# Kernel tuning notes

Measured on AMD Instinct MI355X. Metric: run time of the kernel, lower is better.

Reference implementation:

```python
import jax, jax.numpy as jnp
import numpy as np

H, HKV, D, HIDDEN = 32, 8, 128, 4096
G = H // HKV  # GQA group size = 4
ROPE_THETA = 10000.0


def fwht(x):
    """Fast Walsh-Hadamard transform over the last axis (scale=1, like faster_hadamard_transform default)."""
    d = x.shape[-1]
    orig = x.shape
    x = x.reshape(-1, d)
    h = 1
    while h < d:
        x = x.reshape(-1, d // (2 * h), 2, h)
        a, b = x[:, :, 0, :], x[:, :, 1, :]
        x = jnp.stack([a + b, a - b], axis=2).reshape(-1, d)
        h *= 2
    return x.reshape(orig)


def rope(x, pos):
    """NeoX-style (rotate-half) RoPE at scalar position `pos`; x: [..., D]."""
    half = D // 2
    inv_freq = 1.0 / (ROPE_THETA ** (jnp.arange(0, D, 2, dtype=jnp.float32) / D))  # [half]
    ang = jnp.float32(pos) * inv_freq
    cos, sin = jnp.cos(ang), jnp.sin(ang)
    x1, x2 = x[..., :half], x[..., half:]
    return jnp.concatenate([x1 * cos - x2 * sin, x2 * cos + x1 * sin], axis=-1)


def quant2bit(x):
    """2-bit quantization of Hadamard-domain vectors: per-vector scale = mean(|x|), codes in {-2,-1,0,1}."""
    s = jnp.mean(jnp.abs(x), axis=-1, keepdims=True) + 1e-6
    code = jnp.clip(jnp.round(x / s), -2.0, 1.0)
    return code, s


def _forward(hidden_states, Wq, Wk, Wv, Wo, k_cache, v_cache, top_k):
    x = hidden_states[0, 0]                                 # [HIDDEN]
    q = (x @ Wq.T).reshape(H, D)
    k = (x @ Wk.T).reshape(HKV, D)
    v = (x @ Wv.T).reshape(HKV, D)
    pos = k_cache.shape[0]                                  # decode position (cache len before append)
    q = rope(q, pos)
    k = rope(k, pos)
    # append to cache -> total T = S + 1 tokens
    K = jnp.concatenate([k_cache, k[None]], axis=0)          # [T, HKV, D]
    V = jnp.concatenate([v_cache, v[None]], axis=0)          # [T, HKV, D]
    T = K.shape[0]
    # Hadamard transform + 2-bit codes for estimation
    hq = fwht(q)                                             # [H, D]
    hK = fwht(K)                                             # [T, HKV, D]
    cq, sq = quant2bit(hq)                                   # [H,D], [H,1]
    ck, sk = quant2bit(hK)                                   # [T,HKV,D], [T,HKV,1]
    # estimated attention scores from low-bit codes, per query head
    est = jnp.einsum('ngd,tnd->ngt', cq.reshape(HKV, G, D), ck).reshape(H, T)
    skh = jnp.repeat(sk[:, :, 0].T, G, axis=0)               # [H, T]
    est = est * sq * skh
    est = est.at[:, -1].set(jnp.inf)                         # always keep the current token
    # top-k index selection per head
    _, idx = jax.lax.top_k(est, top_k)                       # [H, top_k]
    kv_map = jnp.arange(H) // G                              # [H]
    Ksel = K[idx, kv_map[:, None], :]                        # [H, top_k, D]
    Vsel = V[idx, kv_map[:, None], :]                        # [H, top_k, D]
    # sparse attention over selected tokens
    logits = jnp.einsum('hd,hkd->hk', q, Ksel) / jnp.sqrt(jnp.float32(D))
    p = jax.nn.softmax(logits, axis=-1)
    attn = jnp.einsum('hk,hkd->hd', p, Vsel).reshape(HIDDEN)
    return (attn @ Wo.T).reshape(1, 1, HIDDEN)


def setup_inputs() -> dict:
    key = jax.random.key(0)
    ks = jax.random.split(key, 7)
    S = 32767
    w = 1.0 / np.sqrt(HIDDEN)
    return {
        'hidden_states': jax.random.normal(ks[0], (1, 1, HIDDEN), jnp.float32),
        'Wq': jax.random.normal(ks[1], (H * D, HIDDEN), jnp.float32) * w,
        'Wk': jax.random.normal(ks[2], (HKV * D, HIDDEN), jnp.float32) * w,
        'Wv': jax.random.normal(ks[3], (HKV * D, HIDDEN), jnp.float32) * w,
        'Wo': jax.random.normal(ks[4], (HIDDEN, HIDDEN), jnp.float32) * w,
        'k_cache': jax.random.normal(ks[5], (S, HKV, D), jnp.float32),
        'v_cache': jax.random.normal(ks[6], (S, HKV, D), jnp.float32),
        'top_k': 2048,
    }


def reference(hidden_states, Wq, Wk, Wv, Wo, k_cache, v_cache, top_k):
    return _forward(hidden_states, Wq, Wk, Wv, Wo, k_cache, v_cache, top_k)
```

## Files before the change

kernel.cpp:

```cpp
#include <hip/hip_runtime.h>
#include <math.h>


typedef __attribute__((ext_vector_type(4))) float f32x4;

#if defined(__has_builtin)
#if __has_builtin(__builtin_amdgcn_sdot4)
#define HAVE_SDOT4 1
#endif
#endif

__device__ __forceinline__ int dot4(int a, int b, int c) {
#ifdef HAVE_SDOT4
  return __builtin_amdgcn_sdot4(a, b, c, false);
#else
  return c + ((a << 24) >> 24) * ((b << 24) >> 24) +
         (((a << 16) >> 24)) * (((b << 16) >> 24)) +
         (((a << 8) >> 24)) * (((b << 8) >> 24)) + (a >> 24) * (b >> 24);
#endif
}

__device__ __forceinline__ unsigned enc_f32(float f) {
  unsigned u = __float_as_uint(f);
  return (u & 0x80000000u) ? ~u : (u | 0x80000000u);
}

__global__ __launch_bounds__(256) void k_gemv_qkv(
    const float* __restrict__ x, const float* __restrict__ Wq,
    const float* __restrict__ Wk, const float* __restrict__ Wv,
    float* __restrict__ y, unsigned* __restrict__ gz) {
  if (blockIdx.x < 96) {
    const int base = blockIdx.x * 512 + threadIdx.x;
    ((uint4*)gz)[base] = make_uint4(0u, 0u, 0u, 0u);
    ((uint4*)gz)[base + 256] = make_uint4(0u, 0u, 0u, 0u);
  }
  const int lane = threadIdx.x & 63;
  const int wid = threadIdx.x >> 6;
  const int row = blockIdx.x * 4 + wid;
  const float* W;
  if (row < 4096) W = Wq + (size_t)row * 4096;
  else if (row < 5120) W = Wk + (size_t)(row - 4096) * 4096;
  else W = Wv + (size_t)(row - 5120) * 4096;
  const float4* W4 = (const float4*)W;
  const float4* x4 = (const float4*)x;
  float acc = 0.f;
#pragma unroll
  for (int i = 0; i < 16; ++i) {
    float4 w = W4[i * 64 + lane];
    float4 xv = x4[i * 64 + lane];
    acc = fmaf(w.x, xv.x, acc);
    acc = fmaf(w.y, xv.y, acc);
    acc = fmaf(w.z, xv.z, acc);
    acc = fmaf(w.w, xv.w, acc);
  }
#pragma unroll
  for (int off = 32; off >= 1; off >>= 1) acc += __shfl_xor(acc, off);
  if (lane == 0) y[row] = acc;
}

__global__ __launch_bounds__(64) void k_rope_quant(
    const float* __restrict__ y, float* __restrict__ q_rope,
    float* __restrict__ k_rope, signed char* __restrict__ cq_i8,
    float* __restrict__ sq, int pos) {
  const int h = blockIdx.x;
  const int lane = threadIdx.x;
  const float* row = (h < 32) ? (y + (size_t)h * 128)
                              : (y + 4096 + (size_t)(h - 32) * 128);
  float x1 = row[lane];
  float x2 = row[lane + 64];
  double e = (double)lane / 64.0;
  float pf = (float)pow(10000.0, e);
  float invf = 1.0f / pf;
  float ang = (float)pos * invf;
  float c = (float)cos((double)ang);
  float s = (float)sin((double)ang);
  float r1 = __fsub_rn(__fmul_rn(x1, c), __fmul_rn(x2, s));
  float r2 = __fadd_rn(__fmul_rn(x2, c), __fmul_rn(x1, s));
  if (h >= 32) {
    k_rope[(size_t)(h - 32) * 128 + lane] = r1;
    k_rope[(size_t)(h - 32) * 128 + 64 + lane] = r2;
    return;
  }
  q_rope[(size_t)h * 128 + lane] = r1;
  q_rope[(size_t)h * 128 + 64 + lane] = r2;
  float a = r1, b = r2;
#pragma unroll
  for (int m = 1; m <= 32; m <<= 1) {
    float ta = __shfl_xor(a, m), tb = __shfl_xor(b, m);
    bool up = (lane & m) == 0;
    a = up ? (a + ta) : (ta - a);
    b = up ? (b + tb) : (tb - b);
  }
  { float na = a + b, nb = a - b; a = na; b = nb; }
  float asum = fabsf(a) + fabsf(b);
#pragma unroll
  for (int m = 32; m >= 1; m >>= 1) asum += __shfl_xor(asum, m);
  float sc = asum * (1.0f / 128.0f) + 1e-6f;
  float ca = fminf(fmaxf(rintf(a / sc), -2.0f), 1.0f);
  float cb = fminf(fmaxf(rintf(b / sc), -2.0f), 1.0f);
  cq_i8[(size_t)h * 128 + lane] = (signed char)(int)ca;
  cq_i8[(size_t)h * 128 + 64 + lane] = (signed char)(int)cb;
  if (lane == 0) sq[h] = sc;
}

__global__ __launch_bounds__(256) void k_quant_est(
    const float* __restrict__ kc, const signed char* __restrict__ cq_i8,
    const float* __restrict__ sq, unsigned* __restrict__ ekeys, int S, int T) {
  const int tid = threadIdx.x;
  const int q = tid & 3;
  const int slot = tid >> 2;
  const int n = blockIdx.y;
  const int t = blockIdx.x * 64 + slot;
  const bool live = t < S;
  const long r = (long)(live ? t : 0) * 8 + n;
  const f32x4* src = (const f32x4*)(kc + r * 128);

  f32x4 G0 = src[q];      f32x4 G1 = src[q + 4];
  f32x4 G2 = src[q + 8];  f32x4 G3 = src[q + 12];
  f32x4 G4 = src[q + 16]; f32x4 G5 = src[q + 20];
  f32x4 G6 = src[q + 24]; f32x4 G7 = src[q + 28];

#define REP8(M) M(G0) M(G1) M(G2) M(G3) M(G4) M(G5) M(G6) M(G7)
#define S1(V) { f32x4 t_ = V; V = (f32x4){t_.x + t_.y, t_.x - t_.y, t_.z + t_.w, t_.z - t_.w}; }
  REP8(S1)
#undef S1
#define S2(V) { f32x4 t_ = V; V = (f32x4){t_.x + t_.z, t_.y + t_.w, t_.x - t_.z, t_.y - t_.w}; }
  REP8(S2)
#undef S2
  {
    const bool up1 = (tid & 1) == 0;
#define XS1(V) { f32x4 t_; t_.x = __shfl_xor(V.x, 1); t_.y = __shfl_xor(V.y, 1); \
                 t_.z = __shfl_xor(V.z, 1); t_.w = __shfl_xor(V.w, 1); \
                 V = up1 ? (V + t_) : (t_ - V); }
    REP8(XS1)
#undef XS1
    const bool up2 = (tid & 2) == 0;
#define XS2(V) { f32x4 t_; t_.x = __shfl_xor(V.x, 2); t_.y = __shfl_xor(V.y, 2); \
                 t_.z = __shfl_xor(V.z, 2); t_.w = __shfl_xor(V.w, 2); \
                 V = up2 ? (V + t_) : (t_ - V); }
    REP8(XS2)
#undef XS2
  }
#define BF(A, B) { f32x4 t_ = A; A = t_ + B; B = t_ - B; }
  BF(G0, G1) BF(G2, G3) BF(G4, G5) BF(G6, G7)
  BF(G0, G2) BF(G1, G3) BF(G4, G6) BF(G5, G7)
  BF(G0, G4) BF(G1, G5) BF(G2, G6) BF(G3, G7)
#undef BF

  f32x4 sv = (f32x4){0.f, 0.f, 0.f, 0.f};
#define FA(V) sv += (f32x4){fabsf(V.x), fabsf(V.y), fabsf(V.z), fabsf(V.w)};
  REP8(FA)
#undef FA
  float asum = (sv.x + sv.y) + (sv.z + sv.w);
  asum += __shfl_xor(asum, 1);
  asum += __shfl_xor(asum, 2);
  const float sc = asum * (1.0f / 128.0f) + 1e-6f;

  const int* cqw = (const int*)cq_i8;
  const int* cq0 = cqw + (n * 4 + 0) * 32 + q;
  const int* cq1 = cqw + (n * 4 + 1) * 32 + q;
  const int* cq2 = cqw + (n * 4 + 2) * 32 + q;
  const int* cq3 = cqw + (n * 4 + 3) * 32 + q;
  int acc0 = 0, acc1 = 0, acc2 = 0, acc3 = 0;
  int j = 0;
#define QD(V) { \
    int c0 = (int)fminf(fmaxf(rintf(V.x / sc), -2.0f), 1.0f); \
    int c1 = (int)fminf(fmaxf(rintf(V.y / sc), -2.0f), 1.0f); \
    int c2 = (int)fminf(fmaxf(rintf(V.z / sc), -2.0f), 1.0f); \
    int c3 = (int)fminf(fmaxf(rintf(V.w / sc), -2.0f), 1.0f); \
    int word = (c0 & 255) | ((c1 & 255) << 8) | ((c2 & 255) << 16) | ((c3 & 255) << 24); \
    acc0 = dot4(word, cq0[4 * j], acc0); \
    acc1 = dot4(word, cq1[4 * j], acc1); \
    acc2 = dot4(word, cq2[4 * j], acc2); \
    acc3 = dot4(word, cq3[4 * j], acc3); \
    ++j; }
  REP8(QD)
#undef QD
#undef REP8

  acc0 += __shfl_xor(acc0, 1); acc0 += __shfl_xor(acc0, 2);
  acc1 += __shfl_xor(acc1, 1); acc1 += __shfl_xor(acc1, 2);
  acc2 += __shfl_xor(acc2, 1); acc2 += __shfl_xor(acc2, 2);
  acc3 += __shfl_xor(acc3, 1); acc3 += __shfl_xor(acc3, 2);

  int accg = (q == 0) ? acc0 : (q == 1) ? acc1 : (q == 2) ? acc2 : acc3;
  float v = ((float)accg * sq[n * 4 + q]) * sc;
  unsigned key = live ? enc_f32(v) : 0xFF800000u;
  ekeys[(size_t)(n * 4 + q) * T + t] = key;
}

template <int NB>
__device__ __forceinline__ void radix_scan(const unsigned* __restrict__ hrow,
                                           unsigned need_in, unsigned& bsel,
                                           unsigned& need_out) {
  const int lane = threadIdx.x & 63;
  constexpr int PL = NB / 64;
  unsigned b[PL];
  unsigned s = 0u;
  const uint4* bp = (const uint4*)(hrow + lane * PL);
#pragma unroll
  for (int i = 0; i < PL / 4; ++i) {
    uint4 v = bp[i];
    b[4 * i] = v.x; b[4 * i + 1] = v.y; b[4 * i + 2] = v.z; b[4 * i + 3] = v.w;
    s += v.x + v.y + v.z + v.w;
  }
  unsigned inc = s;
#pragma unroll
  for (int off = 1; off < 64; off <<= 1) {
    unsigned tv = __shfl_down(inc, off);
    if (lane + off < 64) inc += tv;
  }
  const unsigned suf = inc - s;
  const bool win = (suf < need_in) && (suf + s >= need_in);
  unsigned bs = 0u, n2 = 0u;
  if (win) {
    unsigned running = suf;
#pragma unroll
    for (int i = PL - 1; i >= 0; --i) {
      unsigned cb = b[i];
      if (running + cb >= need_in) { bs = (unsigned)(lane * PL + i); n2 = need_in - running; break; }
      running += cb;
    }
  }
  unsigned long long mw = __ballot(win);
  int srcl = (int)__builtin_ctzll(mw);
  bsel = __shfl(bs, srcl);
  need_out = __shfl(n2, srcl);
}

__global__ __launch_bounds__(256) void k_hist(
    const unsigned* __restrict__ keys, const unsigned* __restrict__ g0,
    const unsigned* __restrict__ g1, unsigned* __restrict__ gout,
    const int* __restrict__ topk_ptr, int pass, int T) {
  const int h = blockIdx.y, c = blockIdx.x, tid = threadIdx.x;
  __shared__ unsigned lh[2048];
#pragma unroll
  for (int i = 0; i < 8; ++i) lh[tid + 256 * i] = 0u;

  int shift, pshift; unsigned mask;
  if (pass == 0) { shift = 21; mask = 0x7FFu; pshift = 0; }
  else if (pass == 1) { shift = 10; mask = 0x7FFu; pshift = 21; }
  else { shift = 0; mask = 0x3FFu; pshift = 10; }

  unsigned pref = 0u;
  if (pass >= 1) {
    const unsigned K = (unsigned)(*topk_ptr);
    unsigned b, nd;
    radix_scan<2048>(g0 + h * 2048, K, b, nd);
    pref = b;
    if (pass == 2) {
      unsigned b1, n1;
      radix_scan<2048>(g1 + h * 2048, nd, b1, n1);
      pref = (pref << 11) | b1;
    }
  }
  __syncthreads();
  const uint4* row = (const uint4*)(keys + (size_t)h * T + c * 2048);
#pragma unroll
  for (int j = 0; j < 2; ++j) {
    uint4 v = row[tid * 2 + j];
    unsigned u[4] = {v.x, v.y, v.z, v.w};
#pragma unroll
    for (int e = 0; e < 4; ++e) {
      bool ok = (pass == 0) || ((u[e] >> pshift) == pref);
      if (ok) atomicAdd(&lh[(u[e] >> shift) & mask], 1u);
    }
  }
  __syncthreads();
#pragma unroll
  for (int i = 0; i < 8; ++i) {
    unsigned cnt = lh[tid + 256 * i];
    if (cnt) atomicAdd(&gout[h * 2048 + tid + 256 * i], cnt);
  }
}

__global__ __launch_bounds__(256) void k_compact(
    const unsigned* __restrict__ keys, const unsigned* __restrict__ g0,
    const unsigned* __restrict__ g1, const unsigned* __restrict__ g2,
    int* __restrict__ idx_out, const int* __restrict__ topk_ptr, int T) {
  const int h = blockIdx.y, c = blockIdx.x, tid = threadIdx.x;
  const unsigned K = (unsigned)(*topk_ptr);
  unsigned b, need, thr;
  radix_scan<2048>(g0 + h * 2048, K, b, need);
  thr = b;
  radix_scan<2048>(g1 + h * 2048, need, b, need);
  thr = (thr << 11) | b;
  radix_scan<1024>(g2 + h * 2048, need, b, need);
  thr = (thr << 10) | b;
  const unsigned gt_total = K - need;

  const unsigned* rowbase = keys + (size_t)h * T;
  unsigned cg = 0u, ce = 0u;
  for (int i = 0; i < c; ++i) {
    const uint4* ch = (const uint4*)(rowbase + i * 2048);
#pragma unroll
    for (int j = 0; j < 2; ++j) {
      uint4 v = ch[tid * 2 + j];
      cg += (v.x > thr) + (v.y > thr) + (v.z > thr) + (v.w > thr);
      ce += (v.x == thr) + (v.y == thr) + (v.z == thr) + (v.w == thr);
    }
  }
  unsigned red = (cg << 16) | ce;
#pragma unroll
  for (int off = 32; off >= 1; off >>= 1) red += __shfl_xor(red, off);
  __shared__ unsigned wsum[4];
  __shared__ unsigned scn[256];
  if ((tid & 63) == 0) wsum[tid >> 6] = red;
  __syncthreads();
  const unsigned basep = wsum[0] + wsum[1] + wsum[2] + wsum[3];
  const unsigned bg = basep >> 16, be = basep & 0xFFFFu;

  const uint4* row = (const uint4*)(rowbase + c * 2048);
  unsigned u[8];
  {
    uint4 v0 = row[tid * 2], v1 = row[tid * 2 + 1];
    u[0] = v0.x; u[1] = v0.y; u[2] = v0.z; u[3] = v0.w;
    u[4] = v1.x; u[5] = v1.y; u[6] = v1.z; u[7] = v1.w;
  }
  unsigned mcg = 0u, mce = 0u;
#pragma unroll
  for (int e = 0; e < 8; ++e) { mcg += (u[e] > thr); mce += (u[e] == thr); }
  unsigned packed = (mcg << 16) | mce;
  scn[tid] = packed;
  __syncthreads();
#pragma unroll
  for (int off = 1; off < 256; off <<= 1) {
    unsigned v = (tid >= off) ? scn[tid - off] : 0u;
    __syncthreads();
    scn[tid] += v;
    __syncthreads();
  }
  const unsigned excl = scn[tid] - packed;
  unsigned exg = bg + (excl >> 16);
  unsigned exe = be + (excl & 0xFFFFu);
  const unsigned tb = (unsigned)(c * 2048 + tid * 8);
  int* dst = idx_out + (size_t)h * K;
#pragma unroll
  for (int e = 0; e < 8; ++e) {
    if (u[e] > thr) dst[exg++] = (int)(tb + e);
    else if (u[e] == thr) {
      unsigned r = exe++;
      if (r < need) dst[gt_total + r] = (int)(tb + e);
    }
  }
}

#define SPLITS 64
#define PSTR 132
__global__ __launch_bounds__(256) void k_attn(
    const float* __restrict__ kc, const float* __restrict__ vc,
    const float* __restrict__ k_rope, const float* __restrict__ v_new,
    const float* __restrict__ q_rope, const int* __restrict__ idx,
    const int* __restrict__ topk_ptr, float* __restrict__ part, int S) {
  const int lane = threadIdx.x & 63;
  const int wid = threadIdx.x >> 6;
  const int h = blockIdx.x;
  const int split = blockIdx.y;
  const int K = *topk_ptr;
  const int n = h >> 2;
  const int per_block = (K + SPLITS - 1) / SPLITS;
  const int j0 = split * per_block;
  const int j1 = min(K, j0 + per_block);
  const int per_wave = (per_block + 3) >> 2;
  const int base = j0 + wid * per_wave;
  float2 qv = ((const float2*)(q_rope + (size_t)h * 128))[lane];
  float ssum = 0.f, a0 = 0.f, a1 = 0.f;
  const float scl = 0.08838834764831845f;
  for (int b = 0; b < per_wave; b += 4) {
    float2 kk[4], vv[4];
    bool val[4];
#pragma unroll
    for (int u = 0; u < 4; ++u) {
      const int j = base + b + u;
      val[u] = (j < j1) && (base + b + u >= j0);
      int t = val[u] ? idx[(size_t)h * (size_t)K + j] : 0;
      const float* kr = (t < S) ? (kc + ((size_t)t * 8 + n) * 128)
                                : (k_rope + (size_t)n * 128);
      const float* vr = (t < S) ? (vc + ((size_t)t * 8 + n) * 128)
                                : (v_new + (size_t)n * 128);
      kk[u] = ((const float2*)kr)[lane];
      vv[u] = ((const float2*)vr)[lane];
    }
    float d[4];
#pragma unroll
    for (int u = 0; u < 4; ++u) d[u] = fmaf(qv.x, kk[u].x, qv.y * kk[u].y);
#pragma unroll
    for (int mm = 32; mm >= 1; mm >>= 1) {
#pragma unroll
      for (int u = 0; u < 4; ++u) d[u] += __shfl_xor(d[u], mm);
    }
#pragma unroll
    for (int u = 0; u < 4; ++u) {
      float p = val[u] ? expf(d[u] * scl) : 0.f;
      ssum += p;
      a0 = fmaf(p, vv[u].x, a0);
      a1 = fmaf(p, vv[u].y, a1);
    }
  }
  __shared__ float lds[4][129];
  lds[wid][2 * lane] = a0;
  lds[wid][2 * lane + 1] = a1;
  if (lane == 0) lds[wid][128] = ssum;
  __syncthreads();
  float* pp = part + (size_t)(h * SPLITS + split) * PSTR;
  const int tid = threadIdx.x;
  if (tid < 128) {
    float s = lds[0][tid] + lds[1][tid] + lds[2][tid] + lds[3][tid];
    pp[1 + tid] = s;
  } else if (tid == 128) {
    pp[0] = lds[0][128] + lds[1][128] + lds[2][128] + lds[3][128];
  }
}

__global__ __launch_bounds__(128) void k_combine(const float* __restrict__ part,
                                                 float* __restrict__ attn) {
  const int h = blockIdx.x;
  const int tid = threadIdx.x;
  const float* base = part + (size_t)h * SPLITS * PSTR;
  float acc = 0.f, ssum = 0.f;
  for (int s = 0; s < SPLITS; ++s) {
    const float* pp = base + (size_t)s * PSTR;
    acc += pp[1 + tid];
    ssum += pp[0];
  }
  attn[(size_t)h * 128 + tid] = acc / ssum;
}

__global__ __launch_bounds__(256) void k_gemv_out(
    const float* __restrict__ attn, const float* __restrict__ Wo,
    float* __restrict__ out) {
  const int lane = threadIdx.x & 63;
  const int wid = threadIdx.x >> 6;
  const int row = blockIdx.x * 4 + wid;
  const float4* W4 = (const float4*)(Wo + (size_t)row * 4096);
  const float4* x4 = (const float4*)attn;
  float acc = 0.f;
#pragma unroll
  for (int i = 0; i < 16; ++i) {
    float4 w = W4[i * 64 + lane];
    float4 xv = x4[i * 64 + lane];
    acc = fmaf(w.x, xv.x, acc);
    acc = fmaf(w.y, xv.y, acc);
    acc = fmaf(w.z, xv.z, acc);
    acc = fmaf(w.w, xv.w, acc);
  }
#pragma unroll
  for (int off = 32; off >= 1; off >>= 1) acc += __shfl_xor(acc, off);
  if (lane == 0) out[row] = acc;
}

extern "C" void kernel_launch(void* const* d_in, const int* in_sizes, int n_in,
                              void* d_out, int out_size, void* d_ws, size_t ws_size,
                              hipStream_t stream) {
  const float* x  = (const float*)d_in[0];
  const float* Wq = (const float*)d_in[1];
  const float* Wk = (const float*)d_in[2];
  const float* Wv = (const float*)d_in[3];
  const float* Wo = (const float*)d_in[4];
  const float* kc = (const float*)d_in[5];
  const float* vc = (const float*)d_in[6];
  const int* topk_ptr = (const int*)d_in[7];
  const int S = in_sizes[5] / (8 * 128);
  const int T = S + 1;

  float* ws = (float*)d_ws;
  float* y      = ws + 0;
  float* q_rope = ws + 6144;
  float* k_rope = ws + 10240;
  float* sq     = ws + 11264;
  float* attn   = ws + 11328;
  signed char* cq_i8 = (signed char*)(ws + 15424);
  unsigned* ekeys = (unsigned*)(ws + 16448);
  unsigned* ghist = (unsigned*)(ws + 1065024);
  unsigned* g0 = ghist, *g1 = ghist + 65536, *g2 = ghist + 131072;
  int*   idx    = (int*)(ws + 1261632);
  float* part   = ws + 1523776;

  const int chunks = T / 2048;

  k_gemv_qkv<<<1536, 256, 0, stream>>>(x, Wq, Wk, Wv, y, ghist);
  k_rope_quant<<<40, 64, 0, stream>>>(y, q_rope, k_rope, cq_i8, sq, S);
  k_quant_est<<<dim3(T / 64, 8), 256, 0, stream>>>(kc, cq_i8, sq, ekeys, S, T);

  k_hist<<<dim3(chunks, 32), 256, 0, stream>>>(ekeys, g0, g1, g0, topk_ptr, 0, T);
  k_hist<<<dim3(chunks, 32), 256, 0, stream>>>(ekeys, g0, g1, g1, topk_ptr, 1, T);
  k_hist<<<dim3(chunks, 32), 256, 0, stream>>>(ekeys, g0, g1, g2, topk_ptr, 2, T);
  k_compact<<<dim3(chunks, 32), 256, 0, stream>>>(ekeys, g0, g1, g2, idx, topk_ptr, T);

  k_attn<<<dim3(32, SPLITS), 256, 0, stream>>>(kc, vc, k_rope, y + 5120, q_rope,
                                               idx, topk_ptr, part, S);
  k_combine<<<32, 128, 0, stream>>>(part, attn);
  k_gemv_out<<<1024, 256, 0, stream>>>(attn, Wo, (float*)d_out);
}
```

Before: 120.0 us.

## Fuse K-cache Hadamard quantization into QKV GEMV launch, fold first histogram into estimation

The Hadamard transform and 2-bit quantization of the cached keys no longer depend on the query, so they move into the QKV GEMV launch as extra blocks. Those blocks write packed int8 codes and per-vector scales to a workspace, which lets the cache quantization overlap with the weight-bound GEMV. The estimation kernel then only reads the compact codes and does dot4 against a permuted query-code layout. It also builds the first radix histogram with atomics, which removes one k_hist launch. The cost is an extra write and read of the code buffer and global atomic contention on the histogram.

Result: slower. 260.8 us (+117.4%).

```diff
diff --git a/kernel.cpp b/kernel.cpp
--- a/kernel.cpp
+++ b/kernel.cpp
@@ -25,37 +25,115 @@
   return (u & 0x80000000u) ? ~u : (u | 0x80000000u);
 }
 
-__global__ __launch_bounds__(256) void k_gemv_qkv(
+
+__global__ __launch_bounds__(256) void k_mega(
     const float* __restrict__ x, const float* __restrict__ Wq,
     const float* __restrict__ Wk, const float* __restrict__ Wv,
-    float* __restrict__ y, unsigned* __restrict__ gz) {
-  if (blockIdx.x < 96) {
-    const int base = blockIdx.x * 512 + threadIdx.x;
-    ((uint4*)gz)[base] = make_uint4(0u, 0u, 0u, 0u);
-    ((uint4*)gz)[base + 256] = make_uint4(0u, 0u, 0u, 0u);
-  }
-  const int lane = threadIdx.x & 63;
-  const int wid = threadIdx.x >> 6;
-  const int row = blockIdx.x * 4 + wid;
-  const float* W;
-  if (row < 4096) W = Wq + (size_t)row * 4096;
-  else if (row < 5120) W = Wk + (size_t)(row - 4096) * 4096;
-  else W = Wv + (size_t)(row - 5120) * 4096;
-  const float4* W4 = (const float4*)W;
-  const float4* x4 = (const float4*)x;
-  float acc = 0.f;
-#pragma unroll
-  for (int i = 0; i < 16; ++i) {
-    float4 w = W4[i * 64 + lane];
-    float4 xv = x4[i * 64 + lane];
-    acc = fmaf(w.x, xv.x, acc);
-    acc = fmaf(w.y, xv.y, acc);
-    acc = fmaf(w.z, xv.z, acc);
-    acc = fmaf(w.w, xv.w, acc);
-  }
-#pragma unroll
-  for (int off = 32; off >= 1; off >>= 1) acc += __shfl_xor(acc, off);
-  if (lane == 0) y[row] = acc;
+    float* __restrict__ y, unsigned* __restrict__ gz,
+    const float* __restrict__ kc, int* __restrict__ ck,
+    float* __restrict__ sk, int S) {
+  const int bx = blockIdx.x;
+  if (bx < 1536) {
+    if (bx < 96) {
+      const int base = bx * 512 + threadIdx.x;
+      ((uint4*)gz)[base] = make_uint4(0u, 0u, 0u, 0u);
+      ((uint4*)gz)[base + 256] = make_uint4(0u, 0u, 0u, 0u);
+    }
+    const int lane = threadIdx.x & 63;
+    const int wid = threadIdx.x >> 6;
+    const int row = bx * 4 + wid;
+    const float* W;
+    if (row < 4096) W = Wq + (size_t)row * 4096;
+    else if (row < 5120) W = Wk + (size_t)(row - 4096) * 4096;
+    else W = Wv + (size_t)(row - 5120) * 4096;
+    const float4* W4 = (const float4*)W;
+    const float4* x4 = (const float4*)x;
+    float acc = 0.f;
+#pragma unroll
+    for (int i = 0; i < 16; ++i) {
+      float4 w = W4[i * 64 + lane];
+      float4 xv = x4[i * 64 + lane];
+      acc = fmaf(w.x, xv.x, acc);
+      acc = fmaf(w.y, xv.y, acc);
+      acc = fmaf(w.z, xv.z, acc);
+      acc = fmaf(w.w, xv.w, acc);
+    }
+#pragma unroll
+    for (int off = 32; off >= 1; off >>= 1) acc += __shfl_xor(acc, off);
+    if (lane == 0) y[row] = acc;
+    return;
+  }
+
+  const int tid = threadIdx.x;
+  const int q = tid & 3;
+  const int slot = tid >> 2;
+  const long r = (long)(bx - 1536) * 64 + slot;
+  const int R = S * 8;
+  const bool live = r < R;
+  const f32x4* src = (const f32x4*)(kc + (live ? r : 0) * 128);
+
+  f32x4 G0 = src[q];      f32x4 G1 = src[q + 4];
+  f32x4 G2 = src[q + 8];  f32x4 G3 = src[q + 12];
+  f32x4 G4 = src[q + 16]; f32x4 G5 = src[q + 20];
+  f32x4 G6 = src[q + 24]; f32x4 G7 = src[q + 28];
+
+#define REP8(M) M(G0) M(G1) M(G2) M(G3) M(G4) M(G5) M(G6) M(G7)
+#define S1(V) { f32x4 t_ = V; V = (f32x4){t_.x + t_.y, t_.x - t_.y, t_.z + t_.w, t_.z - t_.w}; }
+  REP8(S1)
+#undef S1
+#define S2(V) { f32x4 t_ = V; V = (f32x4){t_.x + t_.z, t_.y + t_.w, t_.x - t_.z, t_.y - t_.w}; }
+  REP8(S2)
+#undef S2
+  {
+    const bool up1 = (tid & 1) == 0;
+#define XS1(V) { f32x4 t_; t_.x = __shfl_xor(V.x, 1); t_.y = __shfl_xor(V.y, 1); \
+                 t_.z = __shfl_xor(V.z, 1); t_.w = __shfl_xor(V.w, 1); \
+                 V = up1 ? (V + t_) : (t_ - V); }
+    REP8(XS1)
+#undef XS1
+    const bool up2 = (tid & 2) == 0;
+#define XS2(V) { f32x4 t_; t_.x = __shfl_xor(V.x, 2); t_.y = __shfl_xor(V.y, 2); \
+                 t_.z = __shfl_xor(V.z, 2); t_.w = __shfl_xor(V.w, 2); \
+                 V = up2 ? (V + t_) : (t_ - V); }
+    REP8(XS2)
+#undef XS2
+  }
+#define BF(A, B) { f32x4 t_ = A; A = t_ + B; B = t_ - B; }
+  BF(G0, G1) BF(G2, G3) BF(G4, G5) BF(G6, G7)
+  BF(G0, G2) BF(G1, G3) BF(G4, G6) BF(G5, G7)
+  BF(G0, G4) BF(G1, G5) BF(G2, G6) BF(G3, G7)
+#undef BF
+
+  f32x4 sv = (f32x4){0.f, 0.f, 0.f, 0.f};
+#define FA(V) sv += (f32x4){fabsf(V.x), fabsf(V.y), fabsf(V.z), fabsf(V.w)};
+  REP8(FA)
+#undef FA
+  float asum = (sv.x + sv.y) + (sv.z + sv.w);
+  asum += __shfl_xor(asum, 1);
+  asum += __shfl_xor(asum, 2);
+  const float sc = asum * (1.0f / 128.0f) + 1e-6f;
+
+  int w[8];
+  int j = 0;
+#define QW(V) { \
+    int c0 = (int)fminf(fmaxf(rintf(V.x / sc), -2.0f), 1.0f); \
+    int c1 = (int)fminf(fmaxf(rintf(V.y / sc), -2.0f), 1.0f); \
+    int c2 = (int)fminf(fmaxf(rintf(V.z / sc), -2.0f), 1.0f); \
+    int c3 = (int)fminf(fmaxf(rintf(V.w / sc), -2.0f), 1.0f); \
+    w[j] = (c0 & 255) | ((c1 & 255) << 8) | ((c2 & 255) << 16) | ((c3 & 255) << 24); \
+    ++j; }
+  REP8(QW)
+#undef QW
+#undef REP8
+
+  if (live) {
+    const int t = (int)(r >> 3);
+    const int n = (int)(r & 7);
+    int* dst = ck + ((size_t)(n * 32768 + t) * 32) + q * 8;
+    ((int4*)dst)[0] = make_int4(w[0], w[1], w[2], w[3]);
+    ((int4*)dst)[1] = make_int4(w[4], w[5], w[6], w[7]);
+    if (q == 0) sk[n * 32768 + t] = sc;
+  }
 }
 
 __global__ __launch_bounds__(64) void k_rope_quant(
@@ -98,95 +176,49 @@
   float sc = asum * (1.0f / 128.0f) + 1e-6f;
   float ca = fminf(fmaxf(rintf(a / sc), -2.0f), 1.0f);
   float cb = fminf(fmaxf(rintf(b / sc), -2.0f), 1.0f);
-  cq_i8[(size_t)h * 128 + lane] = (signed char)(int)ca;
-  cq_i8[(size_t)h * 128 + 64 + lane] = (signed char)(int)cb;
+  const int e1 = lane, e2 = lane + 64;
+  const int p1 = ((e1 >> 2) & 3) * 32 + (e1 >> 4) * 4 + (e1 & 3);
+  const int p2 = ((e2 >> 2) & 3) * 32 + (e2 >> 4) * 4 + (e2 & 3);
+  cq_i8[(size_t)h * 128 + p1] = (signed char)(int)ca;
+  cq_i8[(size_t)h * 128 + p2] = (signed char)(int)cb;
   if (lane == 0) sq[h] = sc;
 }
 
-__global__ __launch_bounds__(256) void k_quant_est(
-    const float* __restrict__ kc, const signed char* __restrict__ cq_i8,
-    const float* __restrict__ sq, unsigned* __restrict__ ekeys, int S, int T) {
+__global__ __launch_bounds__(256) void k_est(
+    const int* __restrict__ ck, const float* __restrict__ sk,
+    const signed char* __restrict__ cq_i8, const float* __restrict__ sq,
+    unsigned* __restrict__ ekeys, unsigned* __restrict__ g0, int S, int T) {
   const int tid = threadIdx.x;
   const int q = tid & 3;
   const int slot = tid >> 2;
   const int n = blockIdx.y;
   const int t = blockIdx.x * 64 + slot;
   const bool live = t < S;
-  const long r = (long)(live ? t : 0) * 8 + n;
-  const f32x4* src = (const f32x4*)(kc + r * 128);
-
-  f32x4 G0 = src[q];      f32x4 G1 = src[q + 4];
-  f32x4 G2 = src[q + 8];  f32x4 G3 = src[q + 12];
-  f32x4 G4 = src[q + 16]; f32x4 G5 = src[q + 20];
-  f32x4 G6 = src[q + 24]; f32x4 G7 = src[q + 28];
-
-#define REP8(M) M(G0) M(G1) M(G2) M(G3) M(G4) M(G5) M(G6) M(G7)
-#define S1(V) { f32x4 t_ = V; V = (f32x4){t_.x + t_.y, t_.x - t_.y, t_.z + t_.w, t_.z - t_.w}; }
-  REP8(S1)
-#undef S1
-#define S2(V) { f32x4 t_ = V; V = (f32x4){t_.x + t_.z, t_.y + t_.w, t_.x - t_.z, t_.y - t_.w}; }
-  REP8(S2)
-#undef S2
-  {
-    const bool up1 = (tid & 1) == 0;
-#define XS1(V) { f32x4 t_; t_.x = __shfl_xor(V.x, 1); t_.y = __shfl_xor(V.y, 1); \
-                 t_.z = __shfl_xor(V.z, 1); t_.w = __shfl_xor(V.w, 1); \
-                 V = up1 ? (V + t_) : (t_ - V); }
-    REP8(XS1)
-#undef XS1
-    const bool up2 = (tid & 2) == 0;
-#define XS2(V) { f32x4 t_; t_.x = __shfl_xor(V.x, 2); t_.y = __shfl_xor(V.y, 2); \
-                 t_.z = __shfl_xor(V.z, 2); t_.w = __shfl_xor(V.w, 2); \
-                 V = up2 ? (V + t_) : (t_ - V); }
-    REP8(XS2)
-#undef XS2
-  }
-#define BF(A, B) { f32x4 t_ = A; A = t_ + B; B = t_ - B; }
-  BF(G0, G1) BF(G2, G3) BF(G4, G5) BF(G6, G7)
-  BF(G0, G2) BF(G1, G3) BF(G4, G6) BF(G5, G7)
-  BF(G0, G4) BF(G1, G5) BF(G2, G6) BF(G3, G7)
-#undef BF
-
-  f32x4 sv = (f32x4){0.f, 0.f, 0.f, 0.f};
-#define FA(V) sv += (f32x4){fabsf(V.x), fabsf(V.y), fabsf(V.z), fabsf(V.w)};
-  REP8(FA)
-#undef FA
-  float asum = (sv.x + sv.y) + (sv.z + sv.w);
-  asum += __shfl_xor(asum, 1);
-  asum += __shfl_xor(asum, 2);
-  const float sc = asum * (1.0f / 128.0f) + 1e-6f;
-
+  const int trow = live ? t : 0;
+  const int4* cp = (const int4*)(ck + (size_t)(n * 32768 + trow) * 32 + q * 8);
+  int4 a0 = cp[0], a1 = cp[1];
+  int w[8] = {a0.x, a0.y, a0.z, a0.w, a1.x, a1.y, a1.z, a1.w};
   const int* cqw = (const int*)cq_i8;
-  const int* cq0 = cqw + (n * 4 + 0) * 32 + q;
-  const int* cq1 = cqw + (n * 4 + 1) * 32 + q;
-  const int* cq2 = cqw + (n * 4 + 2) * 32 + q;
-  const int* cq3 = cqw + (n * 4 + 3) * 32 + q;
   int acc0 = 0, acc1 = 0, acc2 = 0, acc3 = 0;
-  int j = 0;
-#define QD(V) { \
-    int c0 = (int)fminf(fmaxf(rintf(V.x / sc), -2.0f), 1.0f); \
-    int c1 = (int)fminf(fmaxf(rintf(V.y / sc), -2.0f), 1.0f); \
-    int c2 = (int)fminf(fmaxf(rintf(V.z / sc), -2.0f), 1.0f); \
-    int c3 = (int)fminf(fmaxf(rintf(V.w / sc), -2.0f), 1.0f); \
-    int word = (c0 & 255) | ((c1 & 255) << 8) | ((c2 & 255) << 16) | ((c3 & 255) << 24); \
-    acc0 = dot4(word, cq0[4 * j], acc0); \
-    acc1 = dot4(word, cq1[4 * j], acc1); \
-    acc2 = dot4(word, cq2[4 * j], acc2); \
-    acc3 = dot4(word, cq3[4 * j], acc3); \
-    ++j; }
-  REP8(QD)
-#undef QD
-#undef REP8
-
+#pragma unroll
+  for (int i = 0; i < 8; ++i) {
+    int cw = w[i];
+    acc0 = dot4(cw, cqw[(n * 4 + 0) * 32 + q * 8 + i], acc0);
+    acc1 = dot4(cw, cqw[(n * 4 + 1) * 32 + q * 8 + i], acc1);
+    acc2 = dot4(cw, cqw[(n * 4 + 2) * 32 + q * 8 + i], acc2);
+    acc3 = dot4(cw, cqw[(n * 4 + 3) * 32 + q * 8 + i], acc3);
+  }
   acc0 += __shfl_xor(acc0, 1); acc0 += __shfl_xor(acc0, 2);
   acc1 += __shfl_xor(acc1, 1); acc1 += __shfl_xor(acc1, 2);
   acc2 += __shfl_xor(acc2, 1); acc2 += __shfl_xor(acc2, 2);
   acc3 += __shfl_xor(acc3, 1); acc3 += __shfl_xor(acc3, 2);
-
+  const float sc = sk[n * 32768 + trow];
   int accg = (q == 0) ? acc0 : (q == 1) ? acc1 : (q == 2) ? acc2 : acc3;
   float v = ((float)accg * sq[n * 4 + q]) * sc;
   unsigned key = live ? enc_f32(v) : 0xFF800000u;
-  ekeys[(size_t)(n * 4 + q) * T + t] = key;
+  const int hplane = n * 4 + q;
+  ekeys[(size_t)hplane * T + t] = key;
+  atomicAdd(&g0[hplane * 2048 + (key >> 21)], 1u);
 }
 
 template <int NB>
@@ -475,14 +507,16 @@
   unsigned* g0 = ghist, *g1 = ghist + 65536, *g2 = ghist + 131072;
   int*   idx    = (int*)(ws + 1261632);
   float* part   = ws + 1523776;
+  float* sk     = ws + 1794112;
+  int*   ck     = (int*)(ws + 2056256);
 
   const int chunks = T / 2048;
-
-  k_gemv_qkv<<<1536, 256, 0, stream>>>(x, Wq, Wk, Wv, y, ghist);
+  const int nquant = (8 * S + 63) / 64;
+
+  k_mega<<<1536 + nquant, 256, 0, stream>>>(x, Wq, Wk, Wv, y, ghist, kc, ck, sk, S);
   k_rope_quant<<<40, 64, 0, stream>>>(y, q_rope, k_rope, cq_i8, sq, S);
-  k_quant_est<<<dim3(T / 64, 8), 256, 0, stream>>>(kc, cq_i8, sq, ekeys, S, T);
-
-  k_hist<<<dim3(chunks, 32), 256, 0, stream>>>(ekeys, g0, g1, g0, topk_ptr, 0, T);
+  k_est<<<dim3(T / 64, 8), 256, 0, stream>>>(ck, sk, cq_i8, sq, ekeys, g0, S, T);
+
   k_hist<<<dim3(chunks, 32), 256, 0, stream>>>(ekeys, g0, g1, g1, topk_ptr, 1, T);
   k_hist<<<dim3(chunks, 32), 256, 0, stream>>>(ekeys, g0, g1, g2, topk_ptr, 2, T);
   k_compact<<<dim3(chunks, 32), 256, 0, stream>>>(ekeys, g0, g1, g2, idx, topk_ptr, T);
```
